# Performance work log

Measured on AMD Instinct MI355X. Metric: run time of the kernel, lower is better.

Reference implementation:

```python
import jax, jax.numpy as jnp
import numpy as np

VOCAB = 30522
HIDDEN = 768
MAX_POS = 512
N_TYPES = 8
N_HEADS = 4
NHID = 128
LN_EPS = 1e-12
ALPHA = 0.01  # LeakyReLU slope
NEG = -9e15


def setup_inputs() -> dict:
    key = jax.random.key(0)
    ks = jax.random.split(key, 12)
    B, N = 8, 256
    token_ids = jax.random.randint(ks[0], (B, N), 0, VOCAB)
    type_ids = jax.random.randint(ks[1], (B, N), 0, 7)
    synset_ids = jax.random.randint(ks[2], (B, N), 0, 32)
    highway = jax.random.randint(ks[3], (B, N), 0, 2).astype(bool)
    tok_emb = jax.random.normal(ks[4], (VOCAB, HIDDEN), jnp.float32) * 0.02
    type_emb = jax.random.normal(ks[5], (N_TYPES, HIDDEN), jnp.float32) * 0.02
    pos_emb = jax.random.normal(ks[6], (MAX_POS, HIDDEN), jnp.float32) * 0.02
    ln_g = jnp.ones((HIDDEN,), jnp.float32)
    ln_b = jnp.zeros((HIDDEN,), jnp.float32)
    # GAT per-head params, xavier-ish scale
    W = jax.random.normal(ks[7], (N_HEADS, HIDDEN, NHID), jnp.float32) * (1.414 * (2.0 / (HIDDEN + NHID)) ** 0.5)
    a = jax.random.normal(ks[8], (N_HEADS, 2 * NHID), jnp.float32) * (1.414 * (2.0 / (2 * NHID + 1)) ** 0.5)
    out_W = jax.random.normal(ks[9], (VOCAB, N_HEADS * NHID), jnp.float32) * 0.02
    out_b = jnp.zeros((VOCAB,), jnp.float32)
    return {"token_ids": token_ids, "type_ids": type_ids, "synset_ids": synset_ids,
            "highway": highway, "tok_emb": tok_emb, "type_emb": type_emb,
            "pos_emb": pos_emb, "ln_g": ln_g, "ln_b": ln_b, "W": W, "a": a,
            "out_W": out_W, "out_b": out_b}


def _graph_mask(token_ids, type_ids, synset_ids, highway):
    # visibility: same synset, plus directed highway edges by type
    vis = synset_ids[:, :, None] == synset_ids[:, None, :]
    t, hw = type_ids, highway
    s1 = (t == 1) & hw
    s3 = (t == 3) & hw
    d1 = (jnp.isin(t, jnp.array([0, 2, 5]))) & hw
    d3 = (jnp.isin(t, jnp.array([6, 4, 0]))) & hw
    vis = vis | (s1[:, :, None] & d1[:, None, :]) | (s3[:, :, None] & d3[:, None, :])
    not_pad = token_ids != 0  # bert padding_idx == 0
    return vis & not_pad[:, None, :]  # (B,N,N)


def reference(token_ids, type_ids, synset_ids, highway, tok_emb, type_emb,
              pos_emb, ln_g, ln_b, W, a, out_W, out_b):
    B, N = token_ids.shape
    mask = _graph_mask(token_ids, type_ids, synset_ids, highway)
    # TaxoEmbedding (eval mode: no dropout)
    x = tok_emb[token_ids] + type_emb[type_ids] + pos_emb[:N][None]
    mu = jnp.mean(x, axis=-1, keepdims=True)
    var = jnp.mean((x - mu) ** 2, axis=-1, keepdims=True)
    x = (x - mu) * jax.lax.rsqrt(var + LN_EPS) * ln_g + ln_b
    # GAT heads. e[h,b,i,j] = leakyrelu(a1_h . Wh[b,i] + a2_h . Wh[b,j])
    Wh = jnp.einsum('bnd,hdf->hbnf', x, W)  # (H,B,N,F)
    F_ = W.shape[-1]
    a1, a2 = a[:, :F_], a[:, F_:]
    e = (jnp.einsum('hbnf,hf->hbn', Wh, a1)[:, :, :, None]
         + jnp.einsum('hbnf,hf->hbn', Wh, a2)[:, :, None, :])
    e = jnp.where(e > 0, e, ALPHA * e)
    e = jnp.where(mask[None], e, NEG)
    att = jax.nn.softmax(e, axis=2)  # torch softmax(dim=1) on (B,N,N) -> i axis
    hp = jax.nn.elu(jnp.einsum('hbij,hbjf->hbif', att, Wh))  # (H,B,N,F)
    cat = hp.transpose(1, 2, 0, 3).reshape(B, N, -1)  # head-major concat
    out = jax.nn.elu(cat @ out_W.T + out_b)
    return jax.nn.log_softmax(out, axis=-1)
```

## Files before the change

kernel.cpp:

```cpp
#include <hip/hip_runtime.h>
#include <hip/hip_bf16.h>

#define VOCAB 30522
#define VPAD 30720
#define HIDDEN 768
#define NHEADS 4
#define NHID 128
#define ROWS 2048
#define KDIM 512
#define LN_EPS 1e-12f
#define ALPHA_LR 0.01f
#define NEGV -9.0e15f
#define NT256 120

typedef __attribute__((ext_vector_type(8))) short short8;
typedef __attribute__((ext_vector_type(4))) float floatx4;
typedef __attribute__((ext_vector_type(2))) float floatx2;
typedef __attribute__((ext_vector_type(4))) unsigned short ushort4v;
typedef __attribute__((ext_vector_type(8))) unsigned short ushort8v;

static __device__ __forceinline__ unsigned short f2bf(float f) {
  unsigned int u = __float_as_uint(f);
  unsigned int r = u + 0x7fffu + ((u >> 16) & 1u);
  return (unsigned short)(r >> 16);
}

static __device__ __forceinline__ void gload16(const unsigned short* g, unsigned short* l) {
  __builtin_amdgcn_global_load_lds(
      (const __attribute__((address_space(1))) void*)g,
      (__attribute__((address_space(3))) void*)l, 16, 0, 0);
}

__global__ __launch_bounds__(256) void k_prep(const float* __restrict__ out_W,
    unsigned short* __restrict__ owb,
    const float* __restrict__ W, unsigned short* __restrict__ Wt,
    const int* __restrict__ tok, const int* __restrict__ typ,
    const float* __restrict__ tok_emb, const float* __restrict__ type_emb, const float* __restrict__ pos_emb,
    const float* __restrict__ ln_g, const float* __restrict__ ln_b, unsigned short* __restrict__ xout) {
  __shared__ unsigned short T[128][136];
  __shared__ float red[8];
  int bid = blockIdx.x;
  if (bid < 2048) {
    int n4src = (VOCAB * KDIM) / 4, n4tot = (VPAD * KDIM) / 4;
    int i = bid * 256 + threadIdx.x;
    int stride = 2048 * 256;
    for (; i < n4tot; i += stride) {
      ushort4v o = {0, 0, 0, 0};
      if (i < n4src) {
        floatx4 v = reinterpret_cast<const floatx4*>(out_W)[i];
        o.x = f2bf(v.x); o.y = f2bf(v.y); o.z = f2bf(v.z); o.w = f2bf(v.w);
      }
      reinterpret_cast<ushort4v*>(owb)[i] = o;
    }
  } else if (bid < 2072) {
    int b = bid - 2048;
    int h = b & 3, dc = b >> 2;
    int tid = threadIdx.x;
    const float* Wb = W + ((long)h * HIDDEN + dc * 128) * NHID;
    #pragma unroll
    for (int q = 0; q < 16; q++) {
      int idx = q * 256 + tid;
      int d = idx >> 5, f4 = idx & 31;
      floatx4 v = *reinterpret_cast<const floatx4*>(&Wb[(long)d * NHID + f4 * 4]);
      #pragma unroll
      for (int j = 0; j < 4; j++) T[f4 * 4 + j][d] = f2bf(v[j]);
    }
    __syncthreads();
    int f = tid >> 1, rh = tid & 1;
    unsigned short* dst = Wt + (long)(h * 128 + f) * HIDDEN + dc * 128 + rh * 64;
    #pragma unroll
    for (int i = 0; i < 8; i++)
      *reinterpret_cast<ushort8v*>(&dst[i * 8]) =
          *reinterpret_cast<const ushort8v*>(&T[f][rh * 64 + i * 8]);
  } else {
    int row = bid - 2072;
    int n = row & 255;
    int t = tok[row], ty = typ[row];
    const float* te = tok_emb + (long)t * HIDDEN;
    const float* ye = type_emb + (long)ty * HIDDEN;
    const float* pe = pos_emb + (long)n * HIDDEN;
    float v[3]; float s = 0.f, ss = 0.f;
    #pragma unroll
    for (int q = 0; q < 3; q++) {
      int d = threadIdx.x + q * 256;
      float x = te[d] + ye[d] + pe[d];
      v[q] = x; s += x; ss += x * x;
    }
    for (int off = 32; off; off >>= 1) { s += __shfl_down(s, off); ss += __shfl_down(ss, off); }
    int wid = threadIdx.x >> 6;
    if ((threadIdx.x & 63) == 0) { red[wid] = s; red[4 + wid] = ss; }
    __syncthreads();
    if (threadIdx.x == 0) {
      float a = red[0] + red[1] + red[2] + red[3];
      float b2 = red[4] + red[5] + red[6] + red[7];
      float mu = a * (1.0f / 768.0f);
      float var = b2 * (1.0f / 768.0f) - mu * mu;
      red[0] = mu; red[1] = rsqrtf(var + LN_EPS);
    }
    __syncthreads();
    float mu = red[0], rstd = red[1];
    #pragma unroll
    for (int q = 0; q < 3; q++) {
      int d = threadIdx.x + q * 256;
      xout[(long)row * HIDDEN + d] = f2bf((v[q] - mu) * rstd * ln_g[d] + ln_b[d]);
    }
  }
}

__global__ __launch_bounds__(256) void k_wh(const unsigned short* __restrict__ A,
    const unsigned short* __restrict__ Bw, float* __restrict__ Wh) {
  int mt = blockIdx.x & 15, nt = blockIdx.x >> 4;
  int m0 = mt * 128, n0 = nt * 128;
  __shared__ __align__(16) unsigned short Al[2][128 * 64];
  __shared__ __align__(16) unsigned short Bl[2][128 * 64];
  int tid = threadIdx.x;
  int l = tid & 63, wid = tid >> 6;
  int wr = wid >> 1, wc = wid & 1;
  int lrow = l & 15, lgrp = l >> 4;
  floatx4 acc[4][4];
  #pragma unroll
  for (int i = 0; i < 4; i++)
    #pragma unroll
    for (int j = 0; j < 4; j++) acc[i][j] = (floatx4){0.f, 0.f, 0.f, 0.f};
  const unsigned short* Ab = A + (long)m0 * HIDDEN;
  const unsigned short* Bb = Bw + (long)n0 * HIDDEN;

  auto STAGE = [&](int t, int bufi) {
    #pragma unroll
    for (int q = 0; q < 4; q++) {
      int chunk = q * 256 + tid;
      int row = chunk >> 3, kp = chunk & 7, swz = kp ^ (row & 7);
      long off = (long)row * HIDDEN + t * 64 + swz * 8;
      gload16(Ab + off, &Al[bufi][chunk * 8]);
      gload16(Bb + off, &Bl[bufi][chunk * 8]);
    }
  };

  STAGE(0, 0);
  STAGE(1, 1);
  asm volatile("s_waitcnt vmcnt(8)" ::: "memory");
  __builtin_amdgcn_sched_barrier(0);
  __builtin_amdgcn_s_barrier();

  #pragma unroll
  for (int kt = 0; kt < 12; kt++) {
    int cur = kt & 1;
    short8 af[2][4], bf[2][4];
    #pragma unroll
    for (int kk = 0; kk < 2; kk++) {
      int sA = (kk * 4 + lgrp) ^ (lrow & 7);
      #pragma unroll
      for (int mi = 0; mi < 4; mi++)
        af[kk][mi] = *reinterpret_cast<const short8*>(&Al[cur][(wr * 64 + mi * 16 + lrow) * 64 + sA * 8]);
      #pragma unroll
      for (int ni = 0; ni < 4; ni++)
        bf[kk][ni] = *reinterpret_cast<const short8*>(&Bl[cur][(wc * 64 + ni * 16 + lrow) * 64 + sA * 8]);
    }
    asm volatile("s_waitcnt lgkmcnt(0)" ::: "memory");
    __builtin_amdgcn_sched_barrier(0);
    __builtin_amdgcn_s_barrier();
    __builtin_amdgcn_sched_barrier(0);
    if (kt < 10) STAGE(kt + 2, cur);
    #pragma unroll
    for (int kk = 0; kk < 2; kk++)
      #pragma unroll
      for (int mi = 0; mi < 4; mi++)
        #pragma unroll
        for (int ni = 0; ni < 4; ni++)
          acc[mi][ni] = __builtin_amdgcn_mfma_f32_16x16x32_bf16(af[kk][mi], bf[kk][ni], acc[mi][ni], 0, 0, 0);
    if (kt < 10) {
      asm volatile("s_waitcnt vmcnt(8)" ::: "memory");
    } else if (kt == 10) {
      asm volatile("s_waitcnt vmcnt(0)" ::: "memory");
    }
    __builtin_amdgcn_sched_barrier(0);
    if (kt < 11) __builtin_amdgcn_s_barrier();
  }

  #pragma unroll
  for (int mi = 0; mi < 4; mi++) {
    #pragma unroll
    for (int reg = 0; reg < 4; reg++) {
      int row = m0 + wr * 64 + mi * 16 + lgrp * 4 + reg;
      #pragma unroll
      for (int ni = 0; ni < 4; ni++) {
        int c = n0 + wc * 64 + ni * 16 + lrow;
        int h = c >> 7, f = c & 127;
        Wh[((long)h * ROWS + row) * NHID + f] = acc[mi][ni][reg];
      }
    }
  }
}

__device__ __forceinline__ unsigned char mk_flags(int t, int hwv, int tokv) {
  unsigned char fl = 0;
  if (hwv) {
    if (t == 1) fl |= 1;
    if (t == 3) fl |= 2;
    if (t == 0 || t == 2 || t == 5) fl |= 4;
    if (t == 6 || t == 4 || t == 0) fl |= 8;
  }
  if (tokv != 0) fl |= 16;
  return fl;
}

__global__ __launch_bounds__(256) void k_ecol(const int* __restrict__ tok, const int* __restrict__ typ,
    const int* __restrict__ syn, const int* __restrict__ hw,
    const float* __restrict__ Wh, const float* __restrict__ a,
    float* __restrict__ e1, float* __restrict__ e2,
    float* __restrict__ colmax, float* __restrict__ colrs) {
  int h = blockIdx.x >> 3, b = blockIdx.x & 7;
  __shared__ float av[256];
  __shared__ float E1[256]; __shared__ int SY[256]; __shared__ unsigned char FL[256];
  int tid = threadIdx.x;
  int g = b * 256 + tid;
  av[tid] = a[h * 256 + tid];
  FL[tid] = mk_flags(typ[g], hw[g], tok[g]);
  SY[tid] = syn[g];
  __syncthreads();
  const float* wr = Wh + ((long)h * ROWS + g) * NHID;
  float s1 = 0.f, s2 = 0.f;
  #pragma unroll 8
  for (int f = 0; f < 128; f++) { float w = wr[f]; s1 += w * av[f]; s2 += w * av[128 + f]; }
  e1[h * ROWS + g] = s1; e2[h * ROWS + g] = s2;
  E1[tid] = s1;
  __syncthreads();
  float e2j = s2;
  int syj = SY[tid]; unsigned char flj = FL[tid];
  bool npj = flj & 16, d1j = flj & 4, d3j = flj & 8;
  float m = -INFINITY;
  for (int i = 0; i < 256; i++) {
    float e = E1[i] + e2j;
    e = e > 0.f ? e : ALPHA_LR * e;
    unsigned char fli = FL[i];
    bool vis = (SY[i] == syj) || ((fli & 1) && d1j) || ((fli & 2) && d3j);
    float v = (vis && npj) ? e : NEGV;
    m = fmaxf(m, v);
  }
  float s = 0.f;
  for (int i = 0; i < 256; i++) {
    float e = E1[i] + e2j;
    e = e > 0.f ? e : ALPHA_LR * e;
    unsigned char fli = FL[i];
    bool vis = (SY[i] == syj) || ((fli & 1) && d1j) || ((fli & 2) && d3j);
    float v = (vis && npj) ? e : NEGV;
    s += __expf(v - m);
  }
  int idx = (h * 8 + b) * 256 + tid;
  colmax[idx] = m;
  colrs[idx] = 1.0f / s;
}

__global__ __launch_bounds__(256) void k_att(const int* __restrict__ tok, const int* __restrict__ typ,
    const int* __restrict__ syn, const int* __restrict__ hw,
    const float* __restrict__ e1, const float* __restrict__ e2,
    const float* __restrict__ colmax, const float* __restrict__ colrs,
    const float* __restrict__ Wh, unsigned short* __restrict__ cat) {
  int chunk = blockIdx.x & 7; int hb = blockIdx.x >> 3;
  int h = hb >> 3, b = hb & 7;
  __shared__ float E2[256], CM[256], CR[256];
  __shared__ int SY[256]; __shared__ unsigned char FL[256];
  __shared__ float WJ[64][128];
  int tid = threadIdx.x;
  {
    int g = b * 256 + tid;
    FL[tid] = mk_flags(typ[g], hw[g], tok[g]);
    E2[tid] = e2[h * ROWS + g];
    CM[tid] = colmax[hb * 256 + tid];
    CR[tid] = colrs[hb * 256 + tid];
    SY[tid] = syn[g];
  }
  __syncthreads();
  int i = chunk * 32 + (tid >> 3);
  int gi = b * 256 + i;
  float e1i = e1[h * ROWS + gi];
  unsigned char fli = FL[i];
  bool s1i = fli & 1, s3i = fli & 2;
  int syni = SY[i];
  int f0 = tid & 7;
  floatx4 acc4[4];
  #pragma unroll
  for (int k2 = 0; k2 < 4; k2++) acc4[k2] = (floatx4){0.f, 0.f, 0.f, 0.f};
  for (int j0 = 0; j0 < 256; j0 += 64) {
    #pragma unroll
    for (int q = 0; q < 8; q++) {
      int e = tid + q * 256;
      int j = e >> 5, f4 = e & 31;
      *reinterpret_cast<floatx4*>(&WJ[j][f4 * 4]) =
          *reinterpret_cast<const floatx4*>(&Wh[((long)h * ROWS + b * 256 + j0 + j) * NHID + f4 * 4]);
    }
    __syncthreads();
    for (int j = 0; j < 64; j++) {
      int jj = j0 + j;
      unsigned char flj = FL[jj];
      bool vis = (syni == SY[jj]) || (s1i && (flj & 4)) || (s3i && (flj & 8));
      bool msk = vis && (flj & 16);
      float ev = e1i + E2[jj];
      ev = ev > 0.f ? ev : ALPHA_LR * ev;
      float v = msk ? ev : NEGV;
      float w = __expf(v - CM[jj]) * CR[jj];
      #pragma unroll
      for (int k2 = 0; k2 < 4; k2++) {
        floatx4 wv = *reinterpret_cast<const floatx4*>(&WJ[j][(f0 + 8 * k2) * 4]);
        acc4[k2] += wv * w;
      }
    }
    __syncthreads();
  }
  ushort4v* cr4 = reinterpret_cast<ushort4v*>(cat + (long)gi * KDIM + h * NHID);
  #pragma unroll
  for (int k2 = 0; k2 < 4; k2++) {
    ushort4v o4;
    #pragma unroll
    for (int e = 0; e < 4; e++) {
      float v = acc4[k2][e];
      v = v > 0.f ? v : __expf(v) - 1.f;
      o4[e] = f2bf(v);
    }
    cr4[f0 + 8 * k2] = o4;
  }
}

__global__ __launch_bounds__(512, 2) void k_gemm(const unsigned short* __restrict__ A,
    const unsigned short* __restrict__ Bw, const float* __restrict__ bias,
    unsigned short* __restrict__ otmp) {
  int bid = blockIdx.x;
  int lin = (bid & 7) * NT256 + (bid >> 3);
  int mt = lin & 7, nt = lin >> 3;
  int m0 = mt * 256, n0 = nt * 256;
  __shared__ __align__(16) char smem[131072];
  unsigned short (*Al)[256 * 64] = reinterpret_cast<unsigned short (*)[256 * 64]>(smem);
  unsigned short (*Bl)[256 * 64] = reinterpret_cast<unsigned short (*)[256 * 64]>(smem + 65536);
  unsigned short* Cl = reinterpret_cast<unsigned short*>(smem);
  int tid = threadIdx.x;
  int l = tid & 63, wid = tid >> 6;
  int wr = wid >> 2, wc = wid & 3;
  int lrow = l & 15, lgrp = l >> 4;
  floatx4 acc[8][4];
  #pragma unroll
  for (int i = 0; i < 8; i++)
    #pragma unroll
    for (int j = 0; j < 4; j++) acc[i][j] = (floatx4){0.f, 0.f, 0.f, 0.f};
  const unsigned short* Ab = A + (long)m0 * KDIM;
  const unsigned short* Bb = Bw + (long)n0 * KDIM;

  auto STAGE = [&](int t, int bufi) {
    #pragma unroll
    for (int q = 0; q < 4; q++) {
      int chunk = q * 512 + tid;
      int row = chunk >> 3, kp = chunk & 7, swz = kp ^ (row & 7);
      long off = (long)row * KDIM + t * 64 + swz * 8;
      gload16(Ab + off, &Al[bufi][chunk * 8]);
      gload16(Bb + off, &Bl[bufi][chunk * 8]);
    }
  };

  STAGE(0, 0);
  STAGE(1, 1);
  asm volatile("s_waitcnt vmcnt(8)" ::: "memory");
  __builtin_amdgcn_sched_barrier(0);
  __builtin_amdgcn_s_barrier();

  #pragma unroll
  for (int kt = 0; kt < 8; kt++) {
    int cur = kt & 1;
    short8 afr[8];
    short8 bfr[4];
    #pragma unroll
    for (int mi = 0; mi < 4; mi++)
      #pragma unroll
      for (int ks = 0; ks < 2; ks++)
        afr[mi * 2 + ks] = *reinterpret_cast<const short8*>(
            &Al[cur][(wr * 128 + mi * 16 + lrow) * 64 + (((ks * 4 + lgrp) ^ (lrow & 7)) * 8)]);
    #pragma unroll
    for (int ni = 0; ni < 2; ni++)
      #pragma unroll
      for (int ks = 0; ks < 2; ks++)
        bfr[ni * 2 + ks] = *reinterpret_cast<const short8*>(
            &Bl[cur][(wc * 64 + ni * 16 + lrow) * 64 + (((ks * 4 + lgrp) ^ (lrow & 7)) * 8)]);
    #pragma unroll
    for (int ks = 0; ks < 2; ks++)
      #pragma unroll
      for (int mi = 0; mi < 4; mi++)
        #pragma unroll
        for (int ni = 0; ni < 2; ni++)
          acc[mi][ni] = __builtin_amdgcn_mfma_f32_16x16x32_bf16(afr[mi * 2 + ks], bfr[ni * 2 + ks], acc[mi][ni], 0, 0, 0);
    __builtin_amdgcn_sched_barrier(0);
    #pragma unroll
    for (int ni = 0; ni < 2; ni++)
      #pragma unroll
      for (int ks = 0; ks < 2; ks++)
        bfr[ni * 2 + ks] = *reinterpret_cast<const short8*>(
            &Bl[cur][(wc * 64 + (2 + ni) * 16 + lrow) * 64 + (((ks * 4 + lgrp) ^ (lrow & 7)) * 8)]);
    #pragma unroll
    for (int ks = 0; ks < 2; ks++)
      #pragma unroll
      for (int mi = 0; mi < 4; mi++)
        #pragma unroll
        for (int ni = 0; ni < 2; ni++)
          acc[mi][2 + ni] = __builtin_amdgcn_mfma_f32_16x16x32_bf16(afr[mi * 2 + ks], bfr[ni * 2 + ks], acc[mi][2 + ni], 0, 0, 0);
    __builtin_amdgcn_sched_barrier(0);
    #pragma unroll
    for (int mi = 0; mi < 4; mi++)
      #pragma unroll
      for (int ks = 0; ks < 2; ks++)
        afr[mi * 2 + ks] = *reinterpret_cast<const short8*>(
            &Al[cur][(wr * 128 + (4 + mi) * 16 + lrow) * 64 + (((ks * 4 + lgrp) ^ (lrow & 7)) * 8)]);
    #pragma unroll
    for (int ks = 0; ks < 2; ks++)
      #pragma unroll
      for (int mi = 0; mi < 4; mi++)
        #pragma unroll
        for (int ni = 0; ni < 2; ni++)
          acc[4 + mi][2 + ni] = __builtin_amdgcn_mfma_f32_16x16x32_bf16(afr[mi * 2 + ks], bfr[ni * 2 + ks], acc[4 + mi][2 + ni], 0, 0, 0);
    __builtin_amdgcn_sched_barrier(0);
    #pragma unroll
    for (int ni = 0; ni < 2; ni++)
      #pragma unroll
      for (int ks = 0; ks < 2; ks++)
        bfr[ni * 2 + ks] = *reinterpret_cast<const short8*>(
            &Bl[cur][(wc * 64 + ni * 16 + lrow) * 64 + (((ks * 4 + lgrp) ^ (lrow & 7)) * 8)]);
    asm volatile("s_waitcnt lgkmcnt(0)" ::: "memory");
    __builtin_amdgcn_sched_barrier(0);
    __builtin_amdgcn_s_barrier();
    __builtin_amdgcn_sched_barrier(0);
    if (kt < 6) STAGE(kt + 2, cur);
    #pragma unroll
    for (int ks = 0; ks < 2; ks++)
      #pragma unroll
      for (int mi = 0; mi < 4; mi++)
        #pragma unroll
        for (int ni = 0; ni < 2; ni++)
          acc[4 + mi][ni] = __builtin_amdgcn_mfma_f32_16x16x32_bf16(afr[mi * 2 + ks], bfr[ni * 2 + ks], acc[4 + mi][ni], 0, 0, 0);
    if (kt < 6) {
      asm volatile("s_waitcnt vmcnt(8)" ::: "memory");
    } else if (kt == 6) {
      asm volatile("s_waitcnt vmcnt(0)" ::: "memory");
    }
    __builtin_amdgcn_sched_barrier(0);
    if (kt < 7) __builtin_amdgcn_s_barrier();
  }
  float bcol[4];
  #pragma unroll
  for (int ni = 0; ni < 4; ni++) {
    int c = n0 + wc * 64 + ni * 16 + lrow;
    bcol[ni] = (c < VOCAB) ? bias[c] : 0.f;
  }
  #pragma unroll
  for (int mi = 0; mi < 8; mi++)
    #pragma unroll
    for (int ni = 0; ni < 4; ni++)
      #pragma unroll
      for (int reg = 0; reg < 4; reg++) {
        int r = wr * 128 + mi * 16 + lgrp * 4 + reg;
        int c = wc * 64 + ni * 16 + lrow;
        float z = acc[mi][ni][reg] + bcol[ni];
        float o = z > 0.f ? z : __expf(z) - 1.f;
        Cl[r * 256 + c] = f2bf(o);
      }
  __syncthreads();
  #pragma unroll
  for (int it = 0; it < 16; it++) {
    int idx = it * 512 + tid;
    int r = idx >> 5, c8 = (idx & 31) * 8;
    int gc = n0 + c8;
    ushort8v v = *reinterpret_cast<const ushort8v*>(&Cl[r * 256 + c8]);
    unsigned short* orow = otmp + (long)(m0 + r) * 2 * VOCAB;
    if (gc + 8 <= VOCAB) {
      *reinterpret_cast<ushort8v*>(orow + gc) = v;
    } else {
      #pragma unroll
      for (int e = 0; e < 8; e++)
        if (gc + e < VOCAB) orow[gc + e] = v[e];
    }
  }
}

__global__ __launch_bounds__(1024) void k_sub(float* __restrict__ out) {
  int row = blockIdx.x;
  float* rb = out + (long)row * VOCAB;
  const unsigned int* src = reinterpret_cast<const unsigned int*>(rb);
  int tid = threadIdx.x;
  unsigned int v[15];
  float se = 0.f;
  #pragma unroll
  for (int i = 0; i < 15; i++) {
    int p = tid + i * 1024;
    v[i] = (p < VOCAB / 2) ? src[p] : 0u;
  }
  #pragma unroll
  for (int i = 0; i < 15; i++) {
    int p = tid + i * 1024;
    if (p < VOCAB / 2) {
      unsigned int u = v[i];
      float lo = __uint_as_float((u & 0xffffu) << 16);
      float hi = __uint_as_float(u & 0xffff0000u);
      se += __expf(lo) + __expf(hi);
    }
  }
  #pragma unroll
  for (int off = 32; off; off >>= 1) se += __shfl_xor(se, off);
  __shared__ float red[16];
  int wid = tid >> 6;
  if ((tid & 63) == 0) red[wid] = se;
  __syncthreads();
  if (tid < 16) {
    float r = red[tid];
    #pragma unroll
    for (int off = 8; off; off >>= 1) r += __shfl_xor(r, off);
    if (tid == 0) red[0] = logf(r);
  }
  __syncthreads();
  float L = red[0];
  floatx2* dst = reinterpret_cast<floatx2*>(rb);
  #pragma unroll
  for (int i = 0; i < 15; i++) {
    int p = tid + i * 1024;
    if (p < VOCAB / 2) {
      unsigned int u = v[i];
      float lo = __uint_as_float((u & 0xffffu) << 16);
      float hi = __uint_as_float(u & 0xffff0000u);
      floatx2 o; o.x = lo - L; o.y = hi - L;
      dst[p] = o;
    }
  }
}

extern "C" void kernel_launch(void* const* d_in, const int* in_sizes, int n_in,
                              void* d_out, int out_size, void* d_ws, size_t ws_size,
                              hipStream_t stream) {
  const int* tok = (const int*)d_in[0];
  const int* typ = (const int*)d_in[1];
  const int* syn = (const int*)d_in[2];
  const int* hw  = (const int*)d_in[3];
  const float* tok_emb  = (const float*)d_in[4];
  const float* type_emb = (const float*)d_in[5];
  const float* pos_emb  = (const float*)d_in[6];
  const float* ln_g = (const float*)d_in[7];
  const float* ln_b = (const float*)d_in[8];
  const float* W    = (const float*)d_in[9];
  const float* a    = (const float*)d_in[10];
  const float* out_W = (const float*)d_in[11];
  const float* out_b = (const float*)d_in[12];
  float* out = (float*)d_out;
  char* ws = (char*)d_ws;
  unsigned short* xb = (unsigned short*)(ws + 0);
  float* Wh  = (float*)(ws + 3145728);
  float* e1  = (float*)(ws + 7340032);
  float* e2  = (float*)(ws + 7372800);
  float* cm  = (float*)(ws + 7405568);
  float* cs  = (float*)(ws + 7438336);
  unsigned short* cat = (unsigned short*)(ws + 7471104);
  unsigned short* Wt  = (unsigned short*)(ws + 9568256);
  unsigned short* owb = (unsigned short*)(ws + 10354688);

  k_prep<<<4120, 256, 0, stream>>>(out_W, owb, W, Wt, tok, typ,
                                   tok_emb, type_emb, pos_emb, ln_g, ln_b, xb);
  k_wh<<<64, 256, 0, stream>>>(xb, Wt, Wh);
  k_ecol<<<32, 256, 0, stream>>>(tok, typ, syn, hw, Wh, a, e1, e2, cm, cs);
  k_att<<<256, 256, 0, stream>>>(tok, typ, syn, hw, e1, e2, cm, cs, Wh, cat);
  k_gemm<<<8 * NT256, 512, 0, stream>>>(cat, owb, out_b, (unsigned short*)out);
  k_sub<<<2048, 1024, 0, stream>>>(out);
}
```

Before: 301.8 us.

## Fuse row exp-sum into GEMM epilogue and vectorize log-softmax subtraction

The GEMM epilogue now computes per-tile partial sums of exp over each output row and writes them to a workspace. A small new kernel reduces those partials into a per-row log-sum-exp, and the subtraction kernel uses it with 16-byte vector loads and stores. This removes the exp and reduction pass from k_sub and adds a shuffle reduction to the GEMM epilogue plus one extra launch. Summing exp without subtracting a max relies on the ELU-bounded logits staying small.

```diff
diff --git a/kernel.cpp b/kernel.cpp
--- a/kernel.cpp
+++ b/kernel.cpp
@@ -18,6 +18,7 @@
 typedef __attribute__((ext_vector_type(2))) float floatx2;
 typedef __attribute__((ext_vector_type(4))) unsigned short ushort4v;
 typedef __attribute__((ext_vector_type(8))) unsigned short ushort8v;
+typedef __attribute__((ext_vector_type(4))) unsigned int uint4v;
 
 static __device__ __forceinline__ unsigned short f2bf(float f) {
   unsigned int u = __float_as_uint(f);
@@ -323,7 +324,7 @@
 
 __global__ __launch_bounds__(512, 2) void k_gemm(const unsigned short* __restrict__ A,
     const unsigned short* __restrict__ Bw, const float* __restrict__ bias,
-    unsigned short* __restrict__ otmp) {
+    unsigned short* __restrict__ otmp, float* __restrict__ ps) {
   int bid = blockIdx.x;
   int lin = (bid & 7) * NT256 + (bid >> 3);
   int mt = lin & 7, nt = lin >> 3;
@@ -465,6 +466,14 @@
     int r = idx >> 5, c8 = (idx & 31) * 8;
     int gc = n0 + c8;
     ushort8v v = *reinterpret_cast<const ushort8v*>(&Cl[r * 256 + c8]);
+    float se = 0.f;
+    #pragma unroll
+    for (int e = 0; e < 8; e++)
+      if (gc + e < VOCAB)
+        se += __expf(__uint_as_float(((unsigned int)(unsigned short)v[e]) << 16));
+    #pragma unroll
+    for (int off = 1; off < 32; off <<= 1) se += __shfl_xor(se, off);
+    if ((idx & 31) == 0) ps[(long)(m0 + r) * 128 + nt] = se;
     unsigned short* orow = otmp + (long)(m0 + r) * 2 * VOCAB;
     if (gc + 8 <= VOCAB) {
       *reinterpret_cast<ushort8v*>(orow + gc) = v;
@@ -476,52 +485,52 @@
   }
 }
 
-__global__ __launch_bounds__(1024) void k_sub(float* __restrict__ out) {
+__global__ __launch_bounds__(128) void k_lse(const float* __restrict__ ps, float* __restrict__ lse) {
   int row = blockIdx.x;
+  int tid = threadIdx.x;
+  float s = (tid < NT256) ? ps[(long)row * 128 + tid] : 0.f;
+  #pragma unroll
+  for (int off = 1; off < 64; off <<= 1) s += __shfl_xor(s, off);
+  __shared__ float red[2];
+  if ((tid & 63) == 0) red[tid >> 6] = s;
+  __syncthreads();
+  if (tid == 0) lse[row] = logf(red[0] + red[1]);
+}
+
+__global__ __launch_bounds__(1024) void k_sub(float* __restrict__ out, const float* __restrict__ lse) {
+  int row = blockIdx.x;
+  float L = lse[row];
   float* rb = out + (long)row * VOCAB;
-  const unsigned int* src = reinterpret_cast<const unsigned int*>(rb);
+  const uint4v* src4 = reinterpret_cast<const uint4v*>(rb);
   int tid = threadIdx.x;
-  unsigned int v[15];
-  float se = 0.f;
-  #pragma unroll
-  for (int i = 0; i < 15; i++) {
-    int p = tid + i * 1024;
-    v[i] = (p < VOCAB / 2) ? src[p] : 0u;
-  }
-  #pragma unroll
-  for (int i = 0; i < 15; i++) {
-    int p = tid + i * 1024;
-    if (p < VOCAB / 2) {
-      unsigned int u = v[i];
-      float lo = __uint_as_float((u & 0xffffu) << 16);
-      float hi = __uint_as_float(u & 0xffff0000u);
-      se += __expf(lo) + __expf(hi);
-    }
-  }
-  #pragma unroll
-  for (int off = 32; off; off >>= 1) se += __shfl_xor(se, off);
-  __shared__ float red[16];
-  int wid = tid >> 6;
-  if ((tid & 63) == 0) red[wid] = se;
+  uint4v v4[4];
+  #pragma unroll
+  for (int k = 0; k < 4; k++) {
+    int p4 = tid + k * 1024;
+    if (p4 < 3816) v4[k] = src4[p4];
+  }
   __syncthreads();
-  if (tid < 16) {
-    float r = red[tid];
-    #pragma unroll
-    for (int off = 8; off; off >>= 1) r += __shfl_xor(r, off);
-    if (tid == 0) red[0] = logf(r);
-  }
-  __syncthreads();
-  float L = red[0];
-  floatx2* dst = reinterpret_cast<floatx2*>(rb);
-  #pragma unroll
-  for (int i = 0; i < 15; i++) {
-    int p = tid + i * 1024;
-    if (p < VOCAB / 2) {
-      unsigned int u = v[i];
-      float lo = __uint_as_float((u & 0xffffu) << 16);
-      float hi = __uint_as_float(u & 0xffff0000u);
-      floatx2 o; o.x = lo - L; o.y = hi - L;
-      dst[p] = o;
+  floatx4* dst4 = reinterpret_cast<floatx4*>(rb);
+  #pragma unroll
+  for (int k = 0; k < 4; k++) {
+    int p4 = tid + k * 1024;
+    if (p4 < 3815) {
+      uint4v u = v4[k];
+      floatx4 a, b;
+      a.x = __uint_as_float((u.x & 0xffffu) << 16) - L;
+      a.y = __uint_as_float(u.x & 0xffff0000u) - L;
+      a.z = __uint_as_float((u.y & 0xffffu) << 16) - L;
+      a.w = __uint_as_float(u.y & 0xffff0000u) - L;
+      b.x = __uint_as_float((u.z & 0xffffu) << 16) - L;
+      b.y = __uint_as_float(u.z & 0xffff0000u) - L;
+      b.z = __uint_as_float((u.w & 0xffffu) << 16) - L;
+      b.w = __uint_as_float(u.w & 0xffff0000u) - L;
+      dst4[2 * p4] = a;
+      dst4[2 * p4 + 1] = b;
+    } else if (p4 == 3815) {
+      unsigned int u = v4[k].x;
+      rb[30520] = __uint_as_float((u & 0xffffu) << 16) - L;
+      rb[30521] = __uint_as_float(u & 0xffff0000u) - L;
     }
   }
 }
@@ -553,12 +562,15 @@
   unsigned short* cat = (unsigned short*)(ws + 7471104);
   unsigned short* Wt  = (unsigned short*)(ws + 9568256);
   unsigned short* owb = (unsigned short*)(ws + 10354688);
+  float* ps  = (float*)(ws + 41811968);
+  float* lse = (float*)(ws + 42860544);
 
   k_prep<<<4120, 256, 0, stream>>>(out_W, owb, W, Wt, tok, typ,
                                    tok_emb, type_emb, pos_emb, ln_g, ln_b, xb);
   k_wh<<<64, 256, 0, stream>>>(xb, Wt, Wh);
   k_ecol<<<32, 256, 0, stream>>>(tok, typ, syn, hw, Wh, a, e1, e2, cm, cs);
   k_att<<<256, 256, 0, stream>>>(tok, typ, syn, hw, e1, e2, cm, cs, Wh, cat);
-  k_gemm<<<8 * NT256, 512, 0, stream>>>(cat, owb, out_b, (unsigned short*)out);
-  k_sub<<<2048, 1024, 0, stream>>>(out);
-}
+  k_gemm<<<8 * NT256, 512, 0, stream>>>(cat, owb, out_b, (unsigned short*)out, ps);
+  k_lse<<<2048, 128, 0, stream>>>(ps, lse);
+  k_sub<<<2048, 1024, 0, stream>>>(out, lse);
+}
```

New measurement: 313.5 us. +3.9%, slower.
